# Performance work log

Hardware: AMD Instinct MI355X
Metric: run time of the kernel (lower is better)

Reference implementation:

```python
import jax, jax.numpy as jnp
import numpy as np

DIM = 2048
NH = 16
HD = DIM // NH
B = 2
S = 2048
HID = 5632  # multiple_of*ceil(int(2*4*dim/3)/multiple_of)
EPS = 1e-6


def setup_inputs() -> dict:
    key = jax.random.key(0)
    ks = jax.random.split(key, 9)
    sd = 0.02
    x = jax.random.normal(ks[0], (B, S, DIM), jnp.float32)
    wq = jax.random.normal(ks[1], (DIM, DIM), jnp.float32) * sd
    wk = jax.random.normal(ks[2], (DIM, DIM), jnp.float32) * sd
    wv = jax.random.normal(ks[3], (DIM, DIM), jnp.float32) * sd
    wo = jax.random.normal(ks[4], (DIM, DIM), jnp.float32) * sd
    w1 = jax.random.normal(ks[5], (DIM, HID), jnp.float32) * sd
    w2 = jax.random.normal(ks[6], (HID, DIM), jnp.float32) * sd
    w3 = jax.random.normal(ks[7], (DIM, HID), jnp.float32) * sd
    attn_norm_w = jnp.ones((DIM,), jnp.float32)
    ffn_norm_w = jnp.ones((DIM,), jnp.float32)
    # RoPE tables: freqs_cis = exp(i * t * theta_j), theta_j = 10000^(-2j/HD)
    inv_freq = 1.0 / (10000.0 ** (np.arange(0, HD, 2).astype(np.float32) / HD))
    t = np.arange(S, dtype=np.float32)
    ang = np.outer(t, inv_freq)  # [S, HD/2]
    freqs_cos = jnp.asarray(np.cos(ang), jnp.float32)
    freqs_sin = jnp.asarray(np.sin(ang), jnp.float32)
    # causal additive mask [1,1,S,S]
    mask = jnp.triu(jnp.full((S, S), float('-inf'), jnp.float32), k=1)[None, None]
    return dict(x=x, wq=wq, wk=wk, wv=wv, wo=wo, w1=w1, w2=w2, w3=w3,
                attn_norm_w=attn_norm_w, ffn_norm_w=ffn_norm_w,
                freqs_cos=freqs_cos, freqs_sin=freqs_sin, mask=mask)


def _rmsnorm(x, w):
    xf = x.astype(jnp.float32)
    v = jnp.mean(xf * xf, axis=-1, keepdims=True)
    return (xf * jax.lax.rsqrt(v + EPS)).astype(x.dtype) * w


def _rope(t, cos, sin):
    # t: [B,S,H,HD] -> pairs (re, im) on last dim
    tr = t.reshape(*t.shape[:-1], HD // 2, 2)
    re, im = tr[..., 0], tr[..., 1]
    c = cos[None, :, None, :]
    s = sin[None, :, None, :]
    out_re = re * c - im * s
    out_im = re * s + im * c
    return jnp.stack([out_re, out_im], axis=-1).reshape(t.shape)


def reference(x, wq, wk, wv, wo, w1, w2, w3, attn_norm_w, ffn_norm_w,
              freqs_cos, freqs_sin, mask):
    # --- attention sublayer ---
    h_in = _rmsnorm(x, attn_norm_w)
    xq = (h_in @ wq).reshape(B, S, NH, HD)
    xk = (h_in @ wk).reshape(B, S, NH, HD)
    xv = (h_in @ wv).reshape(B, S, NH, HD)
    xq = _rope(xq, freqs_cos, freqs_sin)
    xk = _rope(xk, freqs_cos, freqs_sin)
    scale = 1.0 / jnp.sqrt(jnp.float32(HD))
    scores = jnp.einsum('bqhd,bkhd->bhqk', xq, xk) * scale + mask
    probs = jax.nn.softmax(scores.astype(jnp.float32), axis=-1).astype(xq.dtype)
    attn = jnp.einsum('bhqk,bkhd->bqhd', probs, xv).reshape(B, S, DIM)
    h = x + attn @ wo
    # --- feedforward sublayer (SwiGLU) ---
    f_in = _rmsnorm(h, ffn_norm_w)
    ffn = (jax.nn.silu(f_in @ w1) * (f_in @ w3)) @ w2
    return h + ffn
```

## Files before the change

### kernel.cpp

```cpp
#include <hip/hip_runtime.h>

#define DIMQ 2048
#define NHQ  16
#define HDQ  128
#define BQ   2
#define SQ   2048
#define HIDQ 5632
#define MQ   (BQ * SQ)
#define SC_ATTN 0.08838834764831845f

using u16 = unsigned short;
using u32 = unsigned int;
typedef __attribute__((ext_vector_type(8))) short s16x8;
typedef __attribute__((ext_vector_type(4))) float f32x4;

__device__ __forceinline__ float bf2f(u16 v) {
  union { u32 u; float f; } w; w.u = ((u32)v) << 16; return w.f;
}
__device__ __forceinline__ u16 f2bf(float f) {
  union { float f; u32 u; } w; w.f = f;
  u32 r = w.u + 0x7FFFu + ((w.u >> 16) & 1u);
  return (u16)(r >> 16);
}

__device__ __forceinline__ f32x4 mfma16(s16x8 a, s16x8 b, f32x4 c) {
  return __builtin_amdgcn_mfma_f32_16x16x32_bf16(a, b, c, 0, 0, 0);
}

__device__ __forceinline__ void gl_lds16(const void* g, void* l) {
  __builtin_amdgcn_global_load_lds((const __attribute__((address_space(1))) void*)g,
                                   (__attribute__((address_space(3))) void*)l,
                                   16, 0, 0);
}

#define SBAR()                                   \
  {                                              \
    asm volatile("" ::: "memory");               \
    __builtin_amdgcn_s_barrier();                \
    asm volatile("" ::: "memory");               \
  }

__global__ __launch_bounds__(256) void transpose_cvt(const float* __restrict__ src,
                                                     u16* __restrict__ dst,
                                                     int R, int Cn) {
  __shared__ float tile[32][33];
  const int tx = threadIdx.x, ty = threadIdx.y;
  const int c0 = blockIdx.x * 32, r0 = blockIdx.y * 32;
#pragma unroll
  for (int i = 0; i < 4; ++i)
    tile[ty + i * 8][tx] = src[(size_t)(r0 + ty + i * 8) * Cn + c0 + tx];
  __syncthreads();
#pragma unroll
  for (int i = 0; i < 4; ++i)
    dst[(size_t)(c0 + ty + i * 8) * R + r0 + tx] = f2bf(tile[tx][ty + i * 8]);
}

__global__ __launch_bounds__(256) void transpose_cvt_ffn(const float* __restrict__ src,
                                                         u16* __restrict__ dst,
                                                         int base) {
  __shared__ float tile[32][33];
  const int tx = threadIdx.x, ty = threadIdx.y;
  const int c0 = blockIdx.x * 32, r0 = blockIdx.y * 32;
#pragma unroll
  for (int i = 0; i < 4; ++i)
    tile[ty + i * 8][tx] = src[(size_t)(r0 + ty + i * 8) * HIDQ + c0 + tx];
  __syncthreads();
#pragma unroll
  for (int i = 0; i < 4; ++i) {
    const int n = c0 + ty + i * 8;
    const int row = (n >> 7) * 256 + base + (n & 127);
    dst[(size_t)row * DIMQ + r0 + tx] = f2bf(tile[tx][ty + i * 8]);
  }
}

__global__ __launch_bounds__(256) void vtrans_k(const u16* __restrict__ qkv,
                                                u16* __restrict__ vt) {
  __shared__ u16 tile[32][33];
  const int bh = blockIdx.z;
  const int b = bh >> 4, h = bh & 15;
  const int s0 = blockIdx.x * 32, d0 = blockIdx.y * 32;
  const int tx = threadIdx.x, ty = threadIdx.y;
  const u16* src = qkv + (size_t)(b * SQ) * 6144 + 4096 + h * HDQ;
#pragma unroll
  for (int i = 0; i < 4; ++i)
    tile[ty + i * 8][tx] = src[(size_t)(s0 + ty + i * 8) * 6144 + d0 + tx];
  __syncthreads();
  u16* dst = vt + (size_t)bh * HDQ * SQ;
#pragma unroll
  for (int i = 0; i < 4; ++i)
    dst[(size_t)(d0 + ty + i * 8) * SQ + s0 + tx] = tile[tx][ty + i * 8];
}

__global__ __launch_bounds__(256) void rmsnorm_k(const float* __restrict__ x,
                                                 const float* __restrict__ w,
                                                 u16* __restrict__ o) {
  const int row = blockIdx.x;
  const int t = threadIdx.x;
  const float* xr = x + (size_t)row * DIMQ;
  const float4 a = ((const float4*)xr)[t * 2];
  const float4 b = ((const float4*)xr)[t * 2 + 1];
  float ss = a.x * a.x + a.y * a.y + a.z * a.z + a.w * a.w +
             b.x * b.x + b.y * b.y + b.z * b.z + b.w * b.w;
#pragma unroll
  for (int off = 32; off > 0; off >>= 1) ss += __shfl_down(ss, off);
  __shared__ float red[4];
  if ((t & 63) == 0) red[t >> 6] = ss;
  __syncthreads();
  ss = red[0] + red[1] + red[2] + red[3];
  const float rs = rsqrtf(ss * (1.0f / (float)DIMQ) + 1e-6f);
  const float4 wa = ((const float4*)w)[t * 2];
  const float4 wb = ((const float4*)w)[t * 2 + 1];
  s16x8 ov;
  ov[0] = (short)f2bf(a.x * rs * wa.x);
  ov[1] = (short)f2bf(a.y * rs * wa.y);
  ov[2] = (short)f2bf(a.z * rs * wa.z);
  ov[3] = (short)f2bf(a.w * rs * wa.w);
  ov[4] = (short)f2bf(b.x * rs * wb.x);
  ov[5] = (short)f2bf(b.y * rs * wb.y);
  ov[6] = (short)f2bf(b.z * rs * wb.z);
  ov[7] = (short)f2bf(b.w * rs * wb.w);
  *(s16x8*)(o + (size_t)row * DIMQ + t * 8) = ov;
}

template <int OM, int BN, int ROPE>
__global__ __launch_bounds__(512, 1) void gemm256(const u16* __restrict__ A,
                                                  const u16* __restrict__ Bt,
                                                  u16* __restrict__ Cb,
                                                  float* __restrict__ Cf,
                                                  const float* __restrict__ resid,
                                                  const float* __restrict__ fc,
                                                  const float* __restrict__ fs,
                                                  int N, int K, int lda) {
  constexpr int BT = BN * 128;
  constexpr int BLB = BN / 128;
  constexpr int WNv = (BN == 256) ? 4 : 2;
  constexpr int MF = (BN == 256) ? 8 : 4;
  constexpr int MFH = MF / 2;
  __shared__ u16 lds[(65536 + 2 * BT) / 2];
  const int tid = threadIdx.x, wid = tid >> 6, lane = tid & 63;
  const int wm = wid / WNv, wn = wid % WNv;
  const int r = lane & 15, kc = lane >> 4;
  const int nbx = N / BN;
  const int nwg = nbx << 4;
  const int o = blockIdx.x;
  const int seq = (o & 7) * (nwg >> 3) + (o >> 3);
  const int by = seq / nbx, bx = seq - by * nbx;
  const int m0 = by << 8, n0 = bx * BN;
  const int T = K >> 6;

  const u16* Ag = A + (size_t)m0 * lda;
  const u16* Bg = Bt + (size_t)n0 * K;

  const int pl = (tid * 16) ^ (((tid >> 3) & 7) << 4);
  const int prow = pl >> 7;
  const int pcol = (pl & 127) >> 1;

  const int rd0 = r * 128 + ((kc * 16) ^ ((r & 7) << 4));
  const int waveA = wm * (MF * 2048);
  const int waveB = wn * 8192;

  f32x4 acc[MF][4] = {};
  s16x8 af[MFH][2], bfL[2][2], bfH[2][2];

#define STAGE_A(G, kt, BUFB, h)                                                   \
  {                                                                               \
    _Pragma("unroll") for (int i = 0; i < 2; ++i)                                 \
        gl_lds16(G + (size_t)((h) * 128 + i * 64 + prow) * lda + (kt) * 64 + pcol,\
                 (char*)lds + (BUFB) + (h) * 16384 + i * 8192 + (wid << 10));     \
  }
#define STAGE_B(G, kt, BUFB, h)                                                   \
  {                                                                               \
    _Pragma("unroll") for (int i = 0; i < BLB; ++i)                               \
        gl_lds16(G + (size_t)((h) * (BN / 2) + i * 64 + prow) * K + (kt) * 64 + pcol, \
                 (char*)lds + (BUFB) + (h) * (BT / 2) + i * 8192 + (wid << 10));  \
  }

  STAGE_A(Ag, 0, 0, 0);
  STAGE_A(Ag, 0, 0, 1);
  STAGE_B(Bg, 0, 65536, 0);
  STAGE_B(Bg, 0, 65536, 1);
  STAGE_A(Ag, 1, 32768, 0);
  STAGE_A(Ag, 1, 32768, 1);
  asm volatile("s_waitcnt vmcnt(4)" ::: "memory");
  SBAR();

#define TILE_BODY(t, cur)                                                         \
  {                                                                               \
    const int tp1 = ((t) + 1 < T) ? (t) + 1 : T - 1;                              \
    const int tp2 = ((t) + 2 < T) ? (t) + 2 : T - 1;                              \
    const int AB = (cur)*32768;                                                   \
    const int BB = 65536 + (cur)*BT;                                              \
    const int BBn = 65536 + (1 - (cur)) * BT;                                     \
           \
    STAGE_B(Bg, tp1, BBn, 0);                                                     \
    _Pragma("unroll") for (int j = 0; j < MFH; ++j)                               \
        _Pragma("unroll") for (int ks = 0; ks < 2; ++ks)                          \
            af[j][ks] = *(const s16x8*)((const char*)lds + AB + waveA +           \
                                        j * 2048 + (rd0 ^ (ks << 6)));            \
    _Pragma("unroll") for (int n = 0; n < 2; ++n)                                 \
        _Pragma("unroll") for (int ks = 0; ks < 2; ++ks)                          \
            bfL[n][ks] = *(const s16x8*)((const char*)lds + BB + waveB +          \
                                         n * 2048 + (rd0 ^ (ks << 6)));           \
    __builtin_amdgcn_s_setprio(1);                                                \
    _Pragma("unroll") for (int ks = 0; ks < 2; ++ks)                              \
        _Pragma("unroll") for (int j = 0; j < MFH; ++j)                           \
            _Pragma("unroll") for (int n = 0; n < 2; ++n)                         \
                acc[j][n] = mfma16(af[j][ks], bfL[n][ks], acc[j][n]);             \
    __builtin_amdgcn_s_setprio(0);                                                \
                 \
    STAGE_B(Bg, tp1, BBn, 1);                                                     \
    _Pragma("unroll") for (int n = 0; n < 2; ++n)                                 \
        _Pragma("unroll") for (int ks = 0; ks < 2; ++ks)                          \
            bfH[n][ks] = *(const s16x8*)((const char*)lds + BB + waveB +          \
                                         (2 + n) * 2048 + (rd0 ^ (ks << 6)));     \
    __builtin_amdgcn_s_setprio(1);                                                \
    _Pragma("unroll") for (int ks = 0; ks < 2; ++ks)                              \
        _Pragma("unroll") for (int j = 0; j < MFH; ++j)                           \
            _Pragma("unroll") for (int n = 0; n < 2; ++n)                         \
                acc[j][2 + n] = mfma16(af[j][ks], bfH[n][ks], acc[j][2 + n]);     \
    __builtin_amdgcn_s_setprio(0);                                                \
                                  \
    _Pragma("unroll") for (int j = 0; j < MFH; ++j)                               \
        _Pragma("unroll") for (int ks = 0; ks < 2; ++ks)                          \
            af[j][ks] = *(const s16x8*)((const char*)lds + AB + waveA +           \
                                        (MFH + j) * 2048 + (rd0 ^ (ks << 6)));    \
    __builtin_amdgcn_s_setprio(1);                                                \
    _Pragma("unroll") for (int ks = 0; ks < 2; ++ks)                              \
        _Pragma("unroll") for (int j = 0; j < MFH; ++j)                           \
            _Pragma("unroll") for (int n = 0; n < 2; ++n)                         \
                acc[MFH + j][n] = mfma16(af[j][ks], bfL[n][ks], acc[MFH + j][n]); \
    __builtin_amdgcn_s_setprio(0);                                                \
    SBAR();     \
                  \
    STAGE_A(Ag, tp2, AB, 0);                                                      \
    STAGE_A(Ag, tp2, AB, 1);                                                      \
    __builtin_amdgcn_s_setprio(1);                                                \
    _Pragma("unroll") for (int ks = 0; ks < 2; ++ks)                              \
        _Pragma("unroll") for (int j = 0; j < MFH; ++j)                           \
            _Pragma("unroll") for (int n = 0; n < 2; ++n)                         \
                acc[MFH + j][2 + n] = mfma16(af[j][ks], bfH[n][ks], acc[MFH + j][2 + n]); \
    __builtin_amdgcn_s_setprio(0);                                                \
    asm volatile("s_waitcnt vmcnt(4)" ::: "memory");    \
    SBAR();                                                                       \
  }

  for (int tt = 0; tt < T; tt += 2) {
    TILE_BODY(tt, 0);
    TILE_BODY(tt + 1, 1);
  }
#undef TILE_BODY
#undef STAGE_A
#undef STAGE_B

  const bool do_rope = ROPE && (n0 < 4096);
#pragma unroll
  for (int mf = 0; mf < MF; ++mf)
#pragma unroll
    for (int nf = 0; nf < 4; ++nf)
#pragma unroll
      for (int j = 0; j < 4; ++j) {
        const int rr = m0 + wm * (MF * 16) + mf * 16 + kc * 4 + j;
        const int cc = n0 + wn * 64 + nf * 16 + r;
        float v = acc[mf][nf][j];
        if (OM == 0) {
          if (ROPE) {
            const float partner = __shfl_xor(v, 1);
            if (do_rope) {
              const int s = rr & (SQ - 1);
              const int i0 = (cc >> 1) & 63;
              const float cv = fc[s * 64 + i0];
              const float sv = fs[s * 64 + i0];
              v = ((r & 1) == 0) ? v * cv - partner * sv : v * cv + partner * sv;
            }
          }
          Cb[(size_t)rr * N + cc] = f2bf(v);
        } else {
          Cf[(size_t)rr * N + cc] = v + resid[(size_t)rr * N + cc];
        }
      }
}

__global__ __launch_bounds__(512, 1) void gemm_ffn(const u16* __restrict__ A,
                                                   const u16* __restrict__ Bi,
                                                   u16* __restrict__ act) {
  __shared__ u16 lds[65536];
  const int tid = threadIdx.x, wid = tid >> 6, lane = tid & 63;
  const int wm = wid >> 1, wn = wid & 1;
  const int r = lane & 15, kc = lane >> 4;
  const int o = blockIdx.x;
  const int seq = (o & 7) * 88 + (o >> 3);
  const int by = seq / 44, bx = seq - by * 44;
  const int m0 = by << 8;
  const int T = 32;

  const u16* Ag = A + (size_t)m0 * DIMQ;
  const u16* Bg = Bi + (size_t)bx * 256 * DIMQ;

  const int pl = (tid * 16) ^ (((tid >> 3) & 7) << 4);
  const int prow = pl >> 7, pcol = (pl & 127) >> 1;
  const int rd0 = r * 128 + ((kc * 16) ^ ((r & 7) << 4));
  const int waveA = wm * 8192;
  const int waveB = wn * 8192;

  f32x4 accG[4][4] = {}, accU[4][4] = {};
  s16x8 af[4][2], bL[2][2], bH[2][2];

#define STG(G, kt, BUFB, h)                                                       \
  {                                                                               \
    _Pragma("unroll") for (int i = 0; i < 2; ++i)                                 \
        gl_lds16(G + (size_t)((h) * 128 + i * 64 + prow) * DIMQ + (kt) * 64 + pcol,\
                 (char*)lds + (BUFB) + (h) * 16384 + i * 8192 + (wid << 10));     \
  }

  STG(Ag, 0, 0, 0);
  STG(Ag, 0, 0, 1);
  STG(Bg, 0, 65536, 0);
  STG(Bg, 0, 65536, 1);
  STG(Ag, 1, 32768, 0);
  STG(Ag, 1, 32768, 1);
  asm volatile("s_waitcnt vmcnt(4)" ::: "memory");
  SBAR();

#define FFN_BODY(t, cur)                                                          \
  {                                                                               \
    const int tp1 = ((t) + 1 < T) ? (t) + 1 : T - 1;                              \
    const int tp2 = ((t) + 2 < T) ? (t) + 2 : T - 1;                              \
    const int AB = (cur)*32768;                                                   \
    const int BB = 65536 + (cur)*32768;                                           \
    const int BBn = 65536 + (1 - (cur)) * 32768;                                  \
                            \
    STG(Bg, tp1, BBn, 0);                                                         \
    _Pragma("unroll") for (int j = 0; j < 4; ++j)                                 \
        _Pragma("unroll") for (int ks = 0; ks < 2; ++ks)                          \
            af[j][ks] = *(const s16x8*)((const char*)lds + AB + waveA +           \
                                        j * 2048 + (rd0 ^ (ks << 6)));            \
    _Pragma("unroll") for (int n = 0; n < 2; ++n)                                 \
        _Pragma("unroll") for (int ks = 0; ks < 2; ++ks)                          \
            bL[n][ks] = *(const s16x8*)((const char*)lds + BB + waveB +           \
                                        n * 2048 + (rd0 ^ (ks << 6)));            \
    __builtin_amdgcn_s_setprio(1);                                                \
    _Pragma("unroll") for (int ks = 0; ks < 2; ++ks)                              \
        _Pragma("unroll") for (int j = 0; j < 4; ++j)                             \
            _Pragma("unroll") for (int n = 0; n < 2; ++n)                         \
                accG[j][n] = mfma16(af[j][ks], bL[n][ks], accG[j][n]);            \
    __builtin_amdgcn_s_setprio(0);                                                \
                                 \
    STG(Bg, tp1, BBn, 1);                                                         \
    _Pragma("unroll") for (int n = 0; n < 2; ++n)                                 \
        _Pragma("unroll") for (int ks = 0; ks < 2; ++ks)                          \
            bH[n][ks] = *(const s16x8*)((const char*)lds + BB + waveB +           \
                                        (2 + n) * 2048 + (rd0 ^ (ks << 6)));      \
    __builtin_amdgcn_s_setprio(1);                                                \
    _Pragma("unroll") for (int ks = 0; ks < 2; ++ks)                              \
        _Pragma("unroll") for (int j = 0; j < 4; ++j)                             \
            _Pragma("unroll") for (int n = 0; n < 2; ++n)                         \
                accG[j][2 + n] = mfma16(af[j][ks], bH[n][ks], accG[j][2 + n]);    \
    __builtin_amdgcn_s_setprio(0);                                                \
                                                    \
    _Pragma("unroll") for (int n = 0; n < 2; ++n)                                 \
        _Pragma("unroll") for (int ks = 0; ks < 2; ++ks)                          \
            bL[n][ks] = *(const s16x8*)((const char*)lds + BB + 16384 + waveB +   \
                                        n * 2048 + (rd0 ^ (ks << 6)));            \
    __builtin_amdgcn_s_setprio(1);                                                \
    _Pragma("unroll") for (int ks = 0; ks < 2; ++ks)                              \
        _Pragma("unroll") for (int j = 0; j < 4; ++j)                             \
            _Pragma("unroll") for (int n = 0; n < 2; ++n)                         \
                accU[j][n] = mfma16(af[j][ks], bL[n][ks], accU[j][n]);            \
    __builtin_amdgcn_s_setprio(0);                                                \
          \
    _Pragma("unroll") for (int n = 0; n < 2; ++n)                                 \
        _Pragma("unroll") for (int ks = 0; ks < 2; ++ks)                          \
            bH[n][ks] = *(const s16x8*)((const char*)lds + BB + 16384 + waveB +   \
                                        (2 + n) * 2048 + (rd0 ^ (ks << 6)));      \
    SBAR();                        \
                                                 \
    STG(Ag, tp2, AB, 0);                                                          \
    STG(Ag, tp2, AB, 1);                                                          \
    __builtin_amdgcn_s_setprio(1);                                                \
    _Pragma("unroll") for (int ks = 0; ks < 2; ++ks)                              \
        _Pragma("unroll") for (int j = 0; j < 4; ++j)                             \
            _Pragma("unroll") for (int n = 0; n < 2; ++n)                         \
                accU[j][2 + n] = mfma16(af[j][ks], bH[n][ks], accU[j][2 + n]);    \
    __builtin_amdgcn_s_setprio(0);                                                \
    asm volatile("s_waitcnt vmcnt(4)" ::: "memory");                              \
    SBAR();                                                                       \
  }

  for (int tt = 0; tt < T; tt += 2) {
    FFN_BODY(tt, 0);
    FFN_BODY(tt + 1, 1);
  }
#undef FFN_BODY
#undef STG

  const int cbase = bx * 128 + wn * 64;
#pragma unroll
  for (int mf = 0; mf < 4; ++mf)
#pragma unroll
    for (int nf = 0; nf < 4; ++nf)
#pragma unroll
      for (int j = 0; j < 4; ++j) {
        const int rr = m0 + wm * 64 + mf * 16 + kc * 4 + j;
        const int cc = cbase + nf * 16 + r;
        const float g = accG[mf][nf][j];
        const float u = accU[mf][nf][j];
        const float a = g / (1.f + __expf(-g)) * u;
        act[(size_t)rr * HIDQ + cc] = f2bf(a);
      }
}

__global__ __launch_bounds__(256) void attn_k(const u16* __restrict__ qkv,
                                              const u16* __restrict__ vt,
                                              u16* __restrict__ outb) {
  __shared__ u16 Kl[64 * 136];
  __shared__ u16 Vl[128 * 72];
  __shared__ u16 Pl[4][16 * 80];
  const int bh = blockIdx.x;
  const int qt = 31 - blockIdx.y;
  const int b = bh >> 4, h = bh & 15;
  const int q0 = qt * 64;
  const int tid = threadIdx.x, wid = tid >> 6, lane = tid & 63;
  const int r = lane & 15, kc = lane >> 4;
  const size_t base = (size_t)b * SQ * 6144;
  const u16* vtb = vt + (size_t)bh * HDQ * SQ;
  s16x8 qf[4];
  {
    const size_t qoff = base + (size_t)(q0 + wid * 16 + r) * 6144 + h * HDQ;
#pragma unroll
    for (int kk = 0; kk < 4; ++kk)
      qf[kk] = *(const s16x8*)&qkv[qoff + kk * 32 + kc * 8];
  }
  f32x4 acc_o[8] = {};
  float m_run[4], l_run[4];
#pragma unroll
  for (int j = 0; j < 4; ++j) { m_run[j] = -1e30f; l_run[j] = 0.f; }
  const int nt = qt + 1;
  const int skey = tid >> 2, sseg = (tid & 3) * 32;
  const int vd = tid >> 1, vseg = (tid & 1) * 32;
  for (int t = 0; t < nt; ++t) {
    const int kv0 = t * 64;
    __syncthreads();
    {
      const u16* kg = &qkv[base + (size_t)(kv0 + skey) * 6144 + 2048 + h * HDQ + sseg];
      const u16* vg = &vtb[(size_t)vd * SQ + kv0 + vseg];
#pragma unroll
      for (int jj = 0; jj < 4; ++jj)
        *(s16x8*)&Kl[skey * 136 + sseg + jj * 8] = *(const s16x8*)(kg + jj * 8);
#pragma unroll
      for (int jj = 0; jj < 4; ++jj)
        *(s16x8*)&Vl[vd * 72 + vseg + jj * 8] = *(const s16x8*)(vg + jj * 8);
    }
    __syncthreads();
    f32x4 sacc[4] = {};
#pragma unroll
    for (int nf = 0; nf < 4; ++nf)
#pragma unroll
      for (int kk = 0; kk < 4; ++kk) {
        const s16x8 kf = *(const s16x8*)&Kl[(nf * 16 + r) * 136 + kk * 32 + kc * 8];
        sacc[nf] = mfma16(qf[kk], kf, sacc[nf]);
      }
    float p[4][4], alpha[4];
#pragma unroll
    for (int j = 0; j < 4; ++j) {
      const int qrow = q0 + wid * 16 + kc * 4 + j;
      float svs[4];
      float tm = -1e30f;
#pragma unroll
      for (int nf = 0; nf < 4; ++nf) {
        const int key = kv0 + nf * 16 + r;
        float sv = sacc[nf][j] * SC_ATTN;
        sv = (key > qrow) ? -1e30f : sv;
        svs[nf] = sv;
        tm = fmaxf(tm, sv);
      }
      tm = fmaxf(tm, __shfl_xor(tm, 1));
      tm = fmaxf(tm, __shfl_xor(tm, 2));
      tm = fmaxf(tm, __shfl_xor(tm, 4));
      tm = fmaxf(tm, __shfl_xor(tm, 8));
      const float mnew = fmaxf(m_run[j], tm);
      alpha[j] = __expf(m_run[j] - mnew);
      m_run[j] = mnew;
      float rs = 0.f;
#pragma unroll
      for (int nf = 0; nf < 4; ++nf) {
        const float pv = __expf(svs[nf] - mnew);
        p[nf][j] = pv;
        rs += pv;
      }
      rs += __shfl_xor(rs, 1);
      rs += __shfl_xor(rs, 2);
      rs += __shfl_xor(rs, 4);
      rs += __shfl_xor(rs, 8);
      l_run[j] = l_run[j] * alpha[j] + rs;
    }
#pragma unroll
    for (int nf = 0; nf < 8; ++nf)
#pragma unroll
      for (int j = 0; j < 4; ++j)
        acc_o[nf][j] *= alpha[j];
#pragma unroll
    for (int nf = 0; nf < 4; ++nf)
#pragma unroll
      for (int j = 0; j < 4; ++j)
        Pl[wid][(kc * 4 + j) * 80 + nf * 16 + r] = f2bf(p[nf][j]);
#pragma unroll
    for (int ks = 0; ks < 2; ++ks) {
      const s16x8 pa = *(const s16x8*)&Pl[wid][r * 80 + ks * 32 + kc * 8];
#pragma unroll
      for (int nf = 0; nf < 8; ++nf) {
        const s16x8 bv = *(const s16x8*)&Vl[(nf * 16 + r) * 72 + ks * 32 + kc * 8];
        acc_o[nf] = mfma16(pa, bv, acc_o[nf]);
      }
    }
  }
#pragma unroll
  for (int j = 0; j < 4; ++j) {
    const float inv = 1.0f / l_run[j];
    const size_t orow = (size_t)(b * SQ + q0 + wid * 16 + kc * 4 + j) * DIMQ + h * HDQ;
#pragma unroll
    for (int nf = 0; nf < 8; ++nf)
      outb[orow + nf * 16 + r] = f2bf(acc_o[nf][j] * inv);
  }
}

extern "C" void kernel_launch(void* const* d_in, const int* in_sizes, int n_in,
                              void* d_out, int out_size, void* d_ws, size_t ws_size,
                              hipStream_t stream) {
  const float* x   = (const float*)d_in[0];
  const float* wq  = (const float*)d_in[1];
  const float* wk  = (const float*)d_in[2];
  const float* wv  = (const float*)d_in[3];
  const float* wo  = (const float*)d_in[4];
  const float* w1  = (const float*)d_in[5];
  const float* w2  = (const float*)d_in[6];
  const float* w3  = (const float*)d_in[7];
  const float* anw = (const float*)d_in[8];
  const float* fnw = (const float*)d_in[9];
  const float* fc  = (const float*)d_in[10];
  const float* fs  = (const float*)d_in[11];
  float* out = (float*)d_out;

  char* ws = (char*)d_ws;
  u16* wqkvT = (u16*)(ws);
  u16* woT   = (u16*)(ws + 25165824);
  u16* w13i  = (u16*)(ws + 25165824 + 8388608);
  u16* w2T   = (u16*)(ws + 25165824 + 8388608 + 46137344);
  u16* hin   = (u16*)(ws + 102760448);
  u16* qkvb  = (u16*)(ws + 119537664);
  u16* act   = qkvb;
  u16* attnb = (u16*)(ws + 119537664 + 50331648);
  u16* vtb   = (u16*)(ws + 119537664 + 50331648 + 16777216);
  float* h = out;

  const dim3 tb(32, 8);
  transpose_cvt<<<dim3(64, 64), tb, 0, stream>>>(wq, wqkvT, 2048, 2048);
  transpose_cvt<<<dim3(64, 64), tb, 0, stream>>>(wk, wqkvT + (size_t)2048 * 2048, 2048, 2048);
  transpose_cvt<<<dim3(64, 64), tb, 0, stream>>>(wv, wqkvT + (size_t)2 * 2048 * 2048, 2048, 2048);
  transpose_cvt<<<dim3(64, 64), tb, 0, stream>>>(wo, woT, 2048, 2048);
  transpose_cvt_ffn<<<dim3(176, 64), tb, 0, stream>>>(w1, w13i, 0);
  transpose_cvt_ffn<<<dim3(176, 64), tb, 0, stream>>>(w3, w13i, 128);
  transpose_cvt<<<dim3(64, 176), tb, 0, stream>>>(w2, w2T, 5632, 2048);

  rmsnorm_k<<<4096, 256, 0, stream>>>(x, anw, hin);
  gemm256<0, 128, 1><<<768, 512, 0, stream>>>(hin, wqkvT, qkvb, nullptr, nullptr, fc, fs, 6144, 2048, 2048);
  vtrans_k<<<dim3(64, 4, 32), tb, 0, stream>>>(qkvb, vtb);
  attn_k<<<dim3(32, 32), 256, 0, stream>>>(qkvb, vtb, attnb);
  gemm256<1, 128, 0><<<256, 512, 0, stream>>>(attnb, woT, nullptr, h, x, nullptr, nullptr, 2048, 2048, 2048);
  rmsnorm_k<<<4096, 256, 0, stream>>>(h, fnw, hin);
  gemm_ffn<<<704, 512, 0, stream>>>(hin, w13i, act);
  gemm256<1, 128, 0><<<256, 512, 0, stream>>>(act, w2T, nullptr, out, h, nullptr, nullptr, 2048, 5632, 5632);
}
```

Measured before the change: 633.1 us.

## Pair causal query tiles per block and register-prefetch next K/V tile

The attention kernel now runs 512 threads per block and pairs query tile pr with tile 31-pr, so each block does the same total causal work and the K/V tiles are shared by both halves. The next K/V tile is prefetched into registers while the current one is being computed. MFMA sections are wrapped in setprio raises. Waves of the low tile sit idle once their causal range ends, and register pressure rises at the larger block size.

```diff
diff --git a/kernel.cpp b/kernel.cpp
--- a/kernel.cpp
+++ b/kernel.cpp
@@ -367,7 +367,7 @@
             _Pragma("unroll") for (int n = 0; n < 2; ++n)                         \
                 accU[j][n] = mfma16(af[j][ks], bL[n][ks], accU[j][n]);            \
     __builtin_amdgcn_s_setprio(0);                                                \
-          \
+                                                             \
     _Pragma("unroll") for (int n = 0; n < 2; ++n)                                 \
         _Pragma("unroll") for (int ks = 0; ks < 2; ++ks)                          \
             bH[n][ks] = *(const s16x8*)((const char*)lds + BB + 16384 + waveB +   \
@@ -409,23 +409,24 @@
       }
 }
 
-__global__ __launch_bounds__(256) void attn_k(const u16* __restrict__ qkv,
+__global__ __launch_bounds__(512) void attn_k(const u16* __restrict__ qkv,
                                               const u16* __restrict__ vt,
                                               u16* __restrict__ outb) {
   __shared__ u16 Kl[64 * 136];
   __shared__ u16 Vl[128 * 72];
-  __shared__ u16 Pl[4][16 * 80];
+  __shared__ u16 Pl[8][16 * 80];
   const int bh = blockIdx.x;
-  const int qt = 31 - blockIdx.y;
+  const int pr = blockIdx.y;
   const int b = bh >> 4, h = bh & 15;
-  const int q0 = qt * 64;
   const int tid = threadIdx.x, wid = tid >> 6, lane = tid & 63;
   const int r = lane & 15, kc = lane >> 4;
+  const int nt_lo = pr + 1, nt = 32 - pr;
+  const int qbase = ((wid < 4) ? pr * 64 : (31 - pr) * 64) + (wid & 3) * 16;
   const size_t base = (size_t)b * SQ * 6144;
   const u16* vtb = vt + (size_t)bh * HDQ * SQ;
   s16x8 qf[4];
   {
-    const size_t qoff = base + (size_t)(q0 + wid * 16 + r) * 6144 + h * HDQ;
+    const size_t qoff = base + (size_t)(qbase + r) * 6144 + h * HDQ;
 #pragma unroll
     for (int kk = 0; kk < 4; ++kk)
       qf[kk] = *(const s16x8*)&qkv[qoff + kk * 32 + kc * 8];
@@ -434,89 +435,103 @@
   float m_run[4], l_run[4];
 #pragma unroll
   for (int j = 0; j < 4; ++j) { m_run[j] = -1e30f; l_run[j] = 0.f; }
-  const int nt = qt + 1;
-  const int skey = tid >> 2, sseg = (tid & 3) * 32;
-  const int vd = tid >> 1, vseg = (tid & 1) * 32;
+  const int kr = tid >> 4, kc8 = (tid & 15) * 8;
+  const int vr = tid >> 3, vc8 = (tid & 7) * 8;
+  const u16* kgp = &qkv[base + (size_t)kr * 6144 + 2048 + h * HDQ + kc8];
+  const u16* vgp = &vtb[(size_t)vr * SQ + vc8];
+  s16x8 kreg[2], vreg[2];
+  kreg[0] = *(const s16x8*)kgp;
+  kreg[1] = *(const s16x8*)(kgp + (size_t)32 * 6144);
+  vreg[0] = *(const s16x8*)vgp;
+  vreg[1] = *(const s16x8*)(vgp + (size_t)64 * SQ);
   for (int t = 0; t < nt; ++t) {
     const int kv0 = t * 64;
     __syncthreads();
-    {
-      const u16* kg = &qkv[base + (size_t)(kv0 + skey) * 6144 + 2048 + h * HDQ + sseg];
-      const u16* vg = &vtb[(size_t)vd * SQ + kv0 + vseg];
-#pragma unroll
-      for (int jj = 0; jj < 4; ++jj)
-        *(s16x8*)&Kl[skey * 136 + sseg + jj * 8] = *(const s16x8*)(kg + jj * 8);
-#pragma unroll
-      for (int jj = 0; jj < 4; ++jj)
-        *(s16x8*)&Vl[vd * 72 + vseg + jj * 8] = *(const s16x8*)(vg + jj * 8);
+    *(s16x8*)&Kl[kr * 136 + kc8] = kreg[0];
+    *(s16x8*)&Kl[(kr + 32) * 136 + kc8] = kreg[1];
+    *(s16x8*)&Vl[vr * 72 + vc8] = vreg[0];
+    *(s16x8*)&Vl[(vr + 64) * 72 + vc8] = vreg[1];
+    __syncthreads();
+    if (t + 1 < nt) {
+      const u16* kg = kgp + (size_t)(kv0 + 64) * 6144;
+      const u16* vg = vgp + (kv0 + 64);
+      kreg[0] = *(const s16x8*)kg;
+      kreg[1] = *(const s16x8*)(kg + (size_t)32 * 6144);
+      vreg[0] = *(const s16x8*)vg;
+      vreg[1] = *(const s16x8*)(vg + (size_t)64 * SQ);
     }
-    __syncthreads();
-    f32x4 sacc[4] = {};
-#pragma unroll
-    for (int nf = 0; nf < 4; ++nf)
-#pragma unroll
-      for (int kk = 0; kk < 4; ++kk) {
-        const s16x8 kf = *(const s16x8*)&Kl[(nf * 16 + r) * 136 + kk * 32 + kc * 8];
-        sacc[nf] = mfma16(qf[kk], kf, sacc[nf]);
+    if (wid >= 4 || t < nt_lo) {
+      f32x4 sacc[4] = {};
+      __builtin_amdgcn_s_setprio(1);
+#pragma unroll
+      for (int nf = 0; nf < 4; ++nf)
+#pragma unroll
+        for (int kk = 0; kk < 4; ++kk) {
+          const s16x8 kf = *(const s16x8*)&Kl[(nf * 16 + r) * 136 + kk * 32 + kc * 8];
+          sacc[nf] = mfma16(qf[kk], kf, sacc[nf]);
+        }
+      __builtin_amdgcn_s_setprio(0);
+      float p[4][4], alpha[4];
+#pragma unroll
+      for (int j = 0; j < 4; ++j) {
+        const int qrow = qbase + kc * 4 + j;
+        float svs[4];
+        float tm = -1e30f;
+#pragma unroll
+        for (int nf = 0; nf < 4; ++nf) {
+          const int key = kv0 + nf * 16 + r;
+          float sv = sacc[nf][j] * SC_ATTN;
+          sv = (key > qrow) ? -1e30f : sv;
+          svs[nf] = sv;
+          tm = fmaxf(tm, sv);
+        }
+        tm = fmaxf(tm, __shfl_xor(tm, 1));
+        tm = fmaxf(tm, __shfl_xor(tm, 2));
+        tm = fmaxf(tm, __shfl_xor(tm, 4));
+        tm = fmaxf(tm, __shfl_xor(tm, 8));
+        const float mnew = fmaxf(m_run[j], tm);
+        alpha[j] = __expf(m_run[j] - mnew);
+        m_run[j] = mnew;
+        float rs = 0.f;
+#pragma unroll
+        for (int nf = 0; nf < 4; ++nf) {
+          const float pv = __expf(svs[nf] - mnew);
+          p[nf][j] = pv;
+          rs += pv;
+        }
+        rs += __shfl_xor(rs, 1);
+        rs += __shfl_xor(rs, 2);
+        rs += __shfl_xor(rs, 4);
+        rs += __shfl_xor(rs, 8);
+        l_run[j] = l_run[j] * alpha[j] + rs;
       }
-    float p[4][4], alpha[4];
-#pragma unroll
-    for (int j = 0; j < 4; ++j) {
-      const int qrow = q0 + wid * 16 + kc * 4 + j;
-      float svs[4];
-      float tm = -1e30f;
-#pragma unroll
-      for (int nf = 0; nf < 4; ++nf) {
-        const int key = kv0 + nf * 16 + r;
-        float sv = sacc[nf][j] * SC_ATTN;
-        sv = (key > qrow) ? -1e30f : sv;
-        svs[nf] = sv;
-        tm = fmaxf(tm, sv);
+#pragma unroll
+      for (int nf = 0; nf < 8; ++nf)
+#pragma unroll
+        for (int j = 0; j < 4; ++j)
+          acc_o[nf][j] *= alpha[j];
+#pragma unroll
+      for (int nf = 0; nf < 4; ++nf)
+#pragma unroll
+        for (int j = 0; j < 4; ++j)
+          Pl[wid][(kc * 4 + j) * 80 + nf * 16 + r] = f2bf(p[nf][j]);
+      __builtin_amdgcn_s_setprio(1);
+#pragma unroll
+      for (int ks = 0; ks < 2; ++ks) {
+        const s16x8 pa = *(const s16x8*)&Pl[wid][r * 80 + ks * 32 + kc * 8];
+#pragma unroll
+        for (int nf = 0; nf < 8; ++nf) {
+          const s16x8 bv = *(const s16x8*)&Vl[(nf * 16 + r) * 72 + ks * 32 + kc * 8];
+          acc_o[nf] = mfma16(pa, bv, acc_o[nf]);
+        }
       }
-      tm = fmaxf(tm, __shfl_xor(tm, 1));
-      tm = fmaxf(tm, __shfl_xor(tm, 2));
-      tm = fmaxf(tm, __shfl_xor(tm, 4));
-      tm = fmaxf(tm, __shfl_xor(tm, 8));
-      const float mnew = fmaxf(m_run[j], tm);
-      alpha[j] = __expf(m_run[j] - mnew);
-      m_run[j] = mnew;
-      float rs = 0.f;
-#pragma unroll
-      for (int nf = 0; nf < 4; ++nf) {
-        const float pv = __expf(svs[nf] - mnew);
-        p[nf][j] = pv;
-        rs += pv;
-      }
-      rs += __shfl_xor(rs, 1);
-      rs += __shfl_xor(rs, 2);
-      rs += __shfl_xor(rs, 4);
-      rs += __shfl_xor(rs, 8);
-      l_run[j] = l_run[j] * alpha[j] + rs;
-    }
-#pragma unroll
-    for (int nf = 0; nf < 8; ++nf)
-#pragma unroll
-      for (int j = 0; j < 4; ++j)
-        acc_o[nf][j] *= alpha[j];
-#pragma unroll
-    for (int nf = 0; nf < 4; ++nf)
-#pragma unroll
-      for (int j = 0; j < 4; ++j)
-        Pl[wid][(kc * 4 + j) * 80 + nf * 16 + r] = f2bf(p[nf][j]);
-#pragma unroll
-    for (int ks = 0; ks < 2; ++ks) {
-      const s16x8 pa = *(const s16x8*)&Pl[wid][r * 80 + ks * 32 + kc * 8];
-#pragma unroll
-      for (int nf = 0; nf < 8; ++nf) {
-        const s16x8 bv = *(const s16x8*)&Vl[(nf * 16 + r) * 72 + ks * 32 + kc * 8];
-        acc_o[nf] = mfma16(pa, bv, acc_o[nf]);
-      }
+      __builtin_amdgcn_s_setprio(0);
     }
   }
 #pragma unroll
   for (int j = 0; j < 4; ++j) {
     const float inv = 1.0f / l_run[j];
-    const size_t orow = (size_t)(b * SQ + q0 + wid * 16 + kc * 4 + j) * DIMQ + h * HDQ;
+    const size_t orow = (size_t)(b * SQ + qbase + kc * 4 + j) * DIMQ + h * HDQ;
 #pragma unroll
     for (int nf = 0; nf < 8; ++nf)
       outb[orow + nf * 16 + r] = f2bf(acc_o[nf][j] * inv);
@@ -564,7 +579,7 @@
   rmsnorm_k<<<4096, 256, 0, stream>>>(x, anw, hin);
   gemm256<0, 128, 1><<<768, 512, 0, stream>>>(hin, wqkvT, qkvb, nullptr, nullptr, fc, fs, 6144, 2048, 2048);
   vtrans_k<<<dim3(64, 4, 32), tb, 0, stream>>>(qkvb, vtb);
-  attn_k<<<dim3(32, 32), 256, 0, stream>>>(qkvb, vtb, attnb);
+  attn_k<<<dim3(32, 16), 512, 0, stream>>>(qkvb, vtb, attnb);
   gemm256<1, 128, 0><<<256, 512, 0, stream>>>(attnb, woT, nullptr, h, x, nullptr, nullptr, 2048, 2048, 2048);
   rmsnorm_k<<<4096, 256, 0, stream>>>(h, fnw, hin);
   gemm_ffn<<<704, 512, 0, stream>>>(hin, w13i, act);
```

Result: no change. 633.7 us (+0.1%).
